# Kernel tuning notes

Hardware: AMD Instinct MI355X
Metric: run time of the kernel (lower is better)

The kernel has to match this reference:

```python
import jax, jax.numpy as jnp
import numpy as np

B, N, C, H, NC, P = 16, 577, 768, 12, 8, 576  # batch, seq(=patches+cls), dim, heads, curves, patches
D = C // H


def setup_inputs() -> dict:
    key = jax.random.key(0)
    ks = jax.random.split(key, 8)
    x = jax.random.normal(ks[0], (B, N, C), jnp.float32)
    qkv_w = jax.random.normal(ks[1], (C, 3 * C), jnp.float32) * 0.02
    proj_w = jax.random.normal(ks[2], (C, C), jnp.float32) * 0.02
    proj_b = jnp.zeros((C,), jnp.float32)
    # learned per-head decay logits; +3 so sigmoid ~0.95 (slow decay, realistic)
    ai_list = jax.random.normal(ks[3], (NC, H), jnp.float32) + 3.0
    mask_weights = jax.random.normal(ks[4], (NC,), jnp.float32) * 0.1 + 1.0 / NC
    normalize = 1.0 + 0.1 * jax.random.normal(ks[5], (H,), jnp.float32)
    # space-filling-curve inverse index permutations (one per curve)
    curve_inds = jnp.stack([
        jax.random.permutation(jax.random.fold_in(ks[6], c), P) for c in range(NC)
    ]).astype(jnp.int32)
    return dict(x=x, qkv_w=qkv_w, proj_w=proj_w, proj_b=proj_b,
                ai_list=ai_list, mask_weights=mask_weights,
                normalize=normalize, curve_inds=curve_inds)


def _build_mask(ai_list, mask_weights, curve_inds):
    # sigmoid(a)^|i-j| gathered by the curve permutation == sigmoid(a)^|ind_i - ind_j|
    a = jax.nn.sigmoid(ai_list)                                  # [NC,H]
    ci = curve_inds.astype(jnp.float32)                          # [NC,P]
    diff = jnp.abs(ci[:, :, None] - ci[:, None, :])              # [NC,P,P]
    Mc = a[:, :, None, None] ** diff[:, None, :, :]              # [NC,H,P,P]
    Mp = jnp.einsum('c,chpq->hpq', mask_weights, Mc)             # weighted sum over curves
    # cls-token row/col: each curve contributes ones -> sum of weights
    sw = jnp.sum(mask_weights)
    M = jnp.pad(Mp, ((0, 0), (1, 0), (1, 0)))                    # [H,N,N]
    M = M.at[:, 0, :].set(sw)
    M = M.at[:, :, 0].set(sw)
    return M


def reference(x, qkv_w, proj_w, proj_b, ai_list, mask_weights, normalize, curve_inds):
    qkv = (x @ qkv_w).reshape(B, N, 3, H, D)
    q = jnp.transpose(qkv[:, :, 0], (0, 2, 1, 3))                # [B,H,N,D]
    k = jnp.transpose(qkv[:, :, 1], (0, 2, 1, 3))
    v = jnp.transpose(qkv[:, :, 2], (0, 2, 1, 3))
    # NOTE: original overwrites self.scale with the bool `scale`=True -> multiply by 1
    attn = jnp.einsum('bhnd,bhmd->bhnm', q, k)                   # [B,H,N,N]
    M = _build_mask(ai_list, mask_weights, curve_inds)           # [H,N,N]
    attn = attn * M[None] * normalize[None, :, None, None]       # method='mul_v1'
    attn = jax.nn.softmax(attn, axis=-1)
    out = jnp.einsum('bhnm,bhmd->bhnd', attn, v)
    out = jnp.transpose(out, (0, 2, 1, 3)).reshape(B, N, C)
    return out @ proj_w + proj_b
```

## Files before the change

### kernel.cpp

```cpp
#include <hip/hip_runtime.h>


typedef _Float16 f16;
typedef _Float16 half8 __attribute__((ext_vector_type(8)));
typedef _Float16 half4 __attribute__((ext_vector_type(4)));
typedef float floatx4 __attribute__((ext_vector_type(4)));

#define DEVINL __device__ __forceinline__

#define Bb 16
#define NN 577
#define CC 768
#define HH 12
#define DD 64
#define MM (Bb * NN)
#define VTLD 584
#define MLD 580
#define CLD 136
#define TLD 264

DEVINL void async_copy16(void* lds, const void* g) {
  __builtin_amdgcn_global_load_lds(
      (const __attribute__((address_space(1))) void*)g,
      (__attribute__((address_space(3))) void*)lds, 16, 0, 0);
}

DEVINL half8 ld_swz(const f16* lds, int row, int chunk) {
  return *(const half8*)(lds + row * 64 + ((chunk ^ (row & 7)) << 3));
}

DEVINL int xcd_swizzle(int orig, int nwg) {
  int q = nwg >> 3, r = nwg & 7;
  int xcd = orig & 7, loc = orig >> 3;
  return (xcd < r ? xcd * (q + 1) : r * (q + 1) + (xcd - r) * q) + loc;
}

__global__ __launch_bounds__(256)
void prep_kernel(const float* __restrict__ x, const float* __restrict__ qkvw,
                 const float* __restrict__ pw, const float* __restrict__ ai,
                 const float* __restrict__ mw, const float* __restrict__ nrm,
                 const int* __restrict__ ci, f16* __restrict__ x_h,
                 f16* __restrict__ w_t, f16* __restrict__ pw_t,
                 float* __restrict__ Mb) {
  __shared__ float shm[32 * 33];
  const int bid = blockIdx.x;
  const int tid = threadIdx.x;
  if (bid < 6924) {
    int i = (bid * 256 + tid) * 4;
    float4 v = *(const float4*)(x + i);
    half4 o = {(f16)v.x, (f16)v.y, (f16)v.z, (f16)v.w};
    *(half4*)(x_h + i) = o;
  } else if (bid < 9228) {
    bool isq = bid < 8652;
    int b2 = bid - (isq ? 6924 : 8652);
    int N3 = isq ? 3 * CC : CC;
    const float* in = isq ? qkvw : pw;
    f16* out = isq ? w_t : pw_t;
    const int k0 = (b2 % 24) * 32, n0 = (b2 / 24) * 32;
    const int tx = tid & 31, ty = tid >> 5;
#pragma unroll
    for (int p = 0; p < 4; ++p)
      shm[(ty + p * 8) * 33 + tx] = in[(size_t)(k0 + ty + p * 8) * N3 + n0 + tx];
    __syncthreads();
#pragma unroll
    for (int p = 0; p < 4; ++p)
      out[(size_t)(n0 + ty + p * 8) * CC + k0 + tx] = (f16)shm[tx * 33 + ty + p * 8];
  } else {
    int b4 = bid - 9228;
    int i = b4 % NN, h = b4 / NN;
    float* la_s = shm; float* wv_s = shm + 8; float* cif = shm + 16;
    float* swn_s = shm + 24;
    if (tid < 8) {
      float av = ai[tid * 12 + h];
      float a = 1.f / (1.f + __expf(-av));
      la_s[tid] = __logf(a);
      wv_s[tid] = mw[tid];
      cif[tid] = (i > 0) ? (float)ci[tid * 576 + (i - 1)] : 0.f;
    }
    if (tid == 0) {
      float s = 0.f;
      for (int c = 0; c < 8; ++c) s += mw[c];
      swn_s[0] = s * nrm[h] * 1.44269504088896f;
    }
    __syncthreads();
    const float nr = nrm[h] * 1.44269504088896f;
    float* row = Mb + ((size_t)h * NN + i) * MLD;
    for (int j = tid; j < NN; j += 256) {
      float val;
      if (i == 0 || j == 0) {
        val = swn_s[0];
      } else {
        float acc = 0.f;
#pragma unroll
        for (int c = 0; c < 8; ++c) {
          float d = fabsf(cif[c] - (float)ci[c * 576 + (j - 1)]);
          acc += wv_s[c] * __expf(la_s[c] * d);
        }
        val = acc * nr;
      }
      row[j] = val;
    }
  }
}

DEVINL void gemm_mainloop(const f16* __restrict__ A, const f16* __restrict__ Bt,
                          int arow0, int brow0, int maxar,
                          f16* SMEM, floatx4 acc[4][4], int tid) {
  const int lane = tid & 63;
  const int wid = tid >> 6;
  const int wr = wid >> 1, wc = wid & 1;
  const int l15 = lane & 15, g = lane >> 4;
  const int r_ = tid >> 3, cp_ = tid & 7;
  const int lc_ = (cp_ ^ (r_ & 7)) << 3;

  auto stage = [&](f16* As, f16* Bs, int k0) {
#pragma unroll
    for (int q = 0; q < 4; ++q) {
      int r = q * 64 + r_;
      int ar = arow0 + r; if (ar > maxar) ar = maxar;
      async_copy16(As + (q * 512 + tid) * 8, A + (size_t)ar * CC + k0 + lc_);
    }
#pragma unroll
    for (int q = 0; q < 2; ++q) {
      int r = q * 64 + r_;
      async_copy16(Bs + (q * 512 + tid) * 8, Bt + (size_t)(brow0 + r) * CC + k0 + lc_);
    }
  };
  auto compute = [&](const f16* As, const f16* Bs) {
#pragma unroll
    for (int kk = 0; kk < 2; ++kk) {
      half8 af[4], bf[4];
#pragma unroll
      for (int mi = 0; mi < 4; ++mi) af[mi] = ld_swz(As, wr * 64 + mi * 16 + l15, kk * 4 + g);
#pragma unroll
      for (int ni = 0; ni < 4; ++ni) bf[ni] = ld_swz(Bs, wc * 64 + ni * 16 + l15, kk * 4 + g);
#pragma unroll
      for (int mi = 0; mi < 4; ++mi)
#pragma unroll
        for (int ni = 0; ni < 4; ++ni)
          acc[mi][ni] = __builtin_amdgcn_mfma_f32_16x16x32_f16(af[mi], bf[ni], acc[mi][ni], 0, 0, 0);
    }
  };

  const int nt = CC / 64;
  stage(SMEM, SMEM + 16384, 0);
#pragma unroll 1
  for (int t = 0; t < nt; ++t) {
    f16* cAs = (t & 1) ? SMEM + 24576 : SMEM;
    f16* cBs = (t & 1) ? SMEM + 40960 : SMEM + 16384;
    f16* nAs = (t & 1) ? SMEM : SMEM + 24576;
    f16* nBs = (t & 1) ? SMEM + 16384 : SMEM + 40960;
    if (t + 1 < nt) {
      stage(nAs, nBs, (t + 1) * 64);
      asm volatile("s_waitcnt vmcnt(6)" ::: "memory");
    } else {
      asm volatile("s_waitcnt vmcnt(0)" ::: "memory");
    }
    __builtin_amdgcn_s_barrier();
    __builtin_amdgcn_sched_barrier(0);
    compute(cAs, cBs);
    __builtin_amdgcn_s_barrier();
  }
}

__global__ __launch_bounds__(512, 2)
void gemm_qkv(const f16* __restrict__ A, const f16* __restrict__ Bt,
              f16* __restrict__ qb, f16* __restrict__ kb, f16* __restrict__ vt) {
  __shared__ __align__(16) f16 SMEM[49152];
  floatx4 acc[4][4] = {};
  const int nwg = 18 * 37;
  const int wgid = xcd_swizzle(blockIdx.y * gridDim.x + blockIdx.x, nwg);
  const int m0 = (wgid / 18) * 256, n0 = (wgid % 18) * 128;
  gemm_mainloop(A, Bt, m0, n0, MM - 1, SMEM, acc, threadIdx.x);
  const int tid = threadIdx.x, lane = tid & 63, wid = tid >> 6;
  const int wr = wid >> 1, wc = wid & 1, l15 = lane & 15, g = lane >> 4;
  const int t = n0 / CC;
  const int h0 = (n0 - t * CC) >> 6;
  if (t < 2) {
#pragma unroll
    for (int mi = 0; mi < 4; ++mi)
#pragma unroll
      for (int ni = 0; ni < 4; ++ni)
#pragma unroll
        for (int r = 0; r < 4; ++r)
          SMEM[(wr * 64 + mi * 16 + 4 * g + r) * CLD + wc * 64 + ni * 16 + l15] =
              (f16)acc[mi][ni][r];
    __syncthreads();
    f16* dst = (t == 0) ? qb : kb;
#pragma unroll
    for (int p = 0; p < 8; ++p) {
      int c = p * 512 + tid;
      int ml = c >> 4, n3c = (c & 15) << 3;
      int mg = m0 + ml;
      if (mg < MM) {
        int b = mg / NN, n = mg - b * NN;
        int h = h0 + (n3c >> 6), d0 = n3c & 63;
        half8 v = *(const half8*)(SMEM + ml * CLD + n3c);
        *(half8*)(dst + ((size_t)(b * HH + h) * NN + n) * DD + d0) = v;
      }
    }
  } else {
#pragma unroll
    for (int mi = 0; mi < 4; ++mi)
#pragma unroll
      for (int ni = 0; ni < 4; ++ni)
#pragma unroll
        for (int r = 0; r < 4; ++r)
          SMEM[(wc * 64 + ni * 16 + l15) * TLD + wr * 64 + mi * 16 + 4 * g + r] =
              (f16)acc[mi][ni][r];
    __syncthreads();
#pragma unroll
    for (int p = 0; p < 8; ++p) {
      int c = p * 512 + tid;
      int n3 = c >> 5, mc = (c & 31) << 3;
      int mg = m0 + mc;
      int h = h0 + (n3 >> 6), d = n3 & 63;
      half8 v = *(const half8*)(SMEM + n3 * TLD + mc);
      int b0 = mg / NN;
      if (mg + 7 < MM && (mg + 7) / NN == b0) {
        *(half8*)(vt + ((size_t)(b0 * HH + h) * DD + d) * VTLD + (mg - b0 * NN)) = v;
      } else {
#pragma unroll
        for (int e = 0; e < 8; ++e) {
          int m2 = mg + e;
          if (m2 < MM) {
            int b = m2 / NN;
            vt[((size_t)(b * HH + h) * DD + d) * VTLD + (m2 - b * NN)] = v[e];
          }
        }
      }
    }
  }
}

__global__ __launch_bounds__(512, 2)
void gemm_proj(const f16* __restrict__ A, const f16* __restrict__ Bt,
               const float* __restrict__ bias, float* __restrict__ out) {
  __shared__ __align__(16) f16 SMEM[49152];
  floatx4 acc[4][4] = {};
  const int nwg = 6 * 37;
  const int wgid = xcd_swizzle(blockIdx.y * gridDim.x + blockIdx.x, nwg);
  const int m0 = (wgid / 6) * 256, n0 = (wgid % 6) * 128;
  gemm_mainloop(A, Bt, m0, n0, MM - 1, SMEM, acc, threadIdx.x);
  const int lane = threadIdx.x & 63, wid = threadIdx.x >> 6;
  const int wr = wid >> 1, wc = wid & 1, l15 = lane & 15, g = lane >> 4;
#pragma unroll
  for (int mi = 0; mi < 4; ++mi)
#pragma unroll
    for (int ni = 0; ni < 4; ++ni)
#pragma unroll
      for (int r = 0; r < 4; ++r) {
        int m = m0 + wr * 64 + mi * 16 + 4 * g + r;
        if (m >= MM) continue;
        int n = n0 + wc * 64 + ni * 16 + l15;
        out[(size_t)m * CC + n] = acc[mi][ni][r] + bias[n];
      }
}

__global__ __launch_bounds__(512, 4)
void attn_kernel(const f16* __restrict__ qb, const f16* __restrict__ kb,
                 const f16* __restrict__ vt, const float* __restrict__ Mb,
                 f16* __restrict__ aout) {
  __shared__ f16 Ks[2][64 * 64];
  __shared__ f16 Vs[2][64 * 64];
  const int D0 = (blockIdx.z * gridDim.y + blockIdx.y) * gridDim.x + blockIdx.x;
  const int wgid = xcd_swizzle(D0, 5 * HH * Bb);
  const int it = wgid % 5;
  const int rem = wgid / 5;
  const int b = rem % Bb, h = rem / Bb;
  const int tid = threadIdx.x, lane = tid & 63, wid = tid >> 6;
  const int l15 = lane & 15, g = lane >> 4;
  const size_t bh = (size_t)b * HH + h;
  const f16* qbh = qb + bh * NN * DD;
  const f16* kbh = kb + bh * NN * DD;
  const f16* vbh = vt + bh * DD * VTLD;
  const float* Mh = Mb + (size_t)h * NN * MLD;
  const int row0w = it * 128 + wid * 16;

  half8 qB0, qB1;
  {
    int qr = row0w + l15; if (qr > NN - 1) qr = NN - 1;
    const f16* qp = qbh + (size_t)qr * DD + g * 8;
    qB0 = *(const half8*)qp;
    qB1 = *(const half8*)(qp + 32);
  }
  const float* Mrow;
  {
    int r0 = row0w + l15; if (r0 > NN - 1) r0 = NN - 1;
    Mrow = Mh + (size_t)r0 * MLD + 4 * g;
  }

  floatx4 acc[4] = {};
  float lsum = 0.f;
  float mrun = -3e38f;

  const int sr_ = tid >> 3, scp_ = tid & 7;
  const int slc_ = (scp_ ^ (sr_ & 7)) << 3;
  auto stage = [&](f16* Kd, f16* Vd, int j0) {
    int j = j0 + sr_; if (j > NN - 1) j = NN - 1;
    async_copy16(Kd + tid * 8, kbh + (size_t)j * DD + slc_);
    async_copy16(Vd + tid * 8, vbh + (size_t)sr_ * VTLD + j0 + slc_);
  };
  auto ldmask = [&](floatx4 m4[4], int j0) {
#pragma unroll
    for (int jt = 0; jt < 4; ++jt)
      m4[jt] = *(const floatx4*)(Mrow + j0 + jt * 16);
  };
  auto compute = [&](const f16* Kc, const f16* Vc, floatx4 m4[4], int j0) {
    floatx4 sf[4];
#pragma unroll
    for (int jt = 0; jt < 4; ++jt) {
      half8 ka0 = ld_swz(Kc, jt * 16 + l15, g);
      half8 ka1 = ld_swz(Kc, jt * 16 + l15, 4 + g);
      floatx4 z = {0.f, 0.f, 0.f, 0.f};
      z = __builtin_amdgcn_mfma_f32_16x16x32_f16(ka0, qB0, z, 0, 0, 0);
      z = __builtin_amdgcn_mfma_f32_16x16x32_f16(ka1, qB1, z, 0, 0, 0);
      sf[jt] = z;
    }
#pragma unroll
    for (int jt = 0; jt < 4; ++jt)
#pragma unroll
      for (int r = 0; r < 4; ++r) sf[jt][r] *= m4[jt][r];
    if (j0 + 64 > NN) {
#pragma unroll
      for (int jt = 0; jt < 4; ++jt)
#pragma unroll
        for (int r = 0; r < 4; ++r)
          if (j0 + jt * 16 + 4 * g + r >= NN) sf[jt][r] = -3e38f;
    }
    float pj[4];
#pragma unroll
    for (int jt = 0; jt < 4; ++jt)
      pj[jt] = fmaxf(fmaxf(sf[jt][0], sf[jt][1]), fmaxf(sf[jt][2], sf[jt][3]));
    float pmax_loc = fmaxf(fmaxf(pj[0], pj[1]), fmaxf(pj[2], pj[3]));
    if (__any(pmax_loc - mrun > 8.f)) {
      float pmax = fmaxf(pmax_loc, __shfl_xor(pmax_loc, 16));
      pmax = fmaxf(pmax, __shfl_xor(pmax, 32));
      float mnew = fmaxf(mrun, pmax);
      float fac = __builtin_amdgcn_exp2f(mrun - mnew);
      mrun = mnew;
      lsum *= fac;
#pragma unroll
      for (int dt = 0; dt < 4; ++dt)
#pragma unroll
        for (int r = 0; r < 4; ++r) acc[dt][r] *= fac;
    }
    half4 pB[4];
    float lsj[4];
#pragma unroll
    for (int jt = 0; jt < 4; ++jt) {
      half4 pb;
      float p0 = __builtin_amdgcn_exp2f(sf[jt][0] - mrun);
      float p1 = __builtin_amdgcn_exp2f(sf[jt][1] - mrun);
      float p2 = __builtin_amdgcn_exp2f(sf[jt][2] - mrun);
      float p3 = __builtin_amdgcn_exp2f(sf[jt][3] - mrun);
      pb[0] = (f16)p0; pb[1] = (f16)p1; pb[2] = (f16)p2; pb[3] = (f16)p3;
      lsj[jt] = (p0 + p1) + (p2 + p3);
      pB[jt] = pb;
    }
    lsum += (lsj[0] + lsj[1]) + (lsj[2] + lsj[3]);
#pragma unroll
    for (int dt = 0; dt < 4; ++dt)
#pragma unroll
      for (int jt = 0; jt < 4; ++jt) {
        int c16 = (jt * 2 + (g >> 1)) ^ (l15 & 7);
        half4 va = *(const half4*)(Vc + (dt * 16 + l15) * 64 + (c16 << 3) + (g & 1) * 4);
        acc[dt] = __builtin_amdgcn_mfma_f32_16x16x16f16(va, pB[jt], acc[dt], 0, 0, 0);
      }
  };

  floatx4 m4A[4], m4B[4];
  stage(Ks[0], Vs[0], 0);
  ldmask(m4A, 0);

#pragma unroll 1
  for (int t = 0; t < 10; t += 2) {
    ldmask(m4B, (t + 1) * 64);
    asm volatile("s_waitcnt vmcnt(4)" ::: "memory");
    __builtin_amdgcn_s_barrier();
    __builtin_amdgcn_sched_barrier(0);
    stage(Ks[1], Vs[1], (t + 1) * 64);
    compute(Ks[0], Vs[0], m4A, t * 64);
    const int j2 = (t + 2 < 10) ? (t + 2) * 64 : 0;
    ldmask(m4A, j2);
    asm volatile("s_waitcnt vmcnt(4)" ::: "memory");
    __builtin_amdgcn_s_barrier();
    __builtin_amdgcn_sched_barrier(0);
    stage(Ks[0], Vs[0], j2);
    compute(Ks[1], Vs[1], m4B, (t + 1) * 64);
  }

  {
    float v = lsum;
    v += __shfl_xor(v, 16);
    v += __shfl_xor(v, 32);
    float linv = 1.f / v;
    int n = row0w + l15;
    if (n < NN) {
#pragma unroll
      for (int dt = 0; dt < 4; ++dt) {
        half4 o;
#pragma unroll
        for (int r = 0; r < 4; ++r) o[r] = (f16)(acc[dt][r] * linv);
        *(half4*)(aout + ((size_t)(b * NN + n)) * CC + h * DD + dt * 16 + 4 * g) = o;
      }
    }
  }
}

extern "C" void kernel_launch(void* const* d_in, const int* in_sizes, int n_in,
                              void* d_out, int out_size, void* d_ws, size_t ws_size,
                              hipStream_t stream) {
  const float* x    = (const float*)d_in[0];
  const float* qkvw = (const float*)d_in[1];
  const float* pw   = (const float*)d_in[2];
  const float* pb   = (const float*)d_in[3];
  const float* ai   = (const float*)d_in[4];
  const float* mw   = (const float*)d_in[5];
  const float* nrm  = (const float*)d_in[6];
  const int*   ci   = (const int*)d_in[7];
  float* out = (float*)d_out;

  char* wsb = (char*)d_ws;
  size_t off = 0;
  auto alloc = [&](size_t bytes) {
    char* p = wsb + off;
    off += (bytes + 255) & ~(size_t)255;
    return p;
  };
  f16*   x_h  = (f16*)alloc((size_t)MM * CC * 2);
  f16*   w_t  = (f16*)alloc((size_t)3 * CC * CC * 2);
  f16*   pw_t = (f16*)alloc((size_t)CC * CC * 2);
  float* Mb   = (float*)alloc((size_t)HH * NN * MLD * 4 + 1024);
  f16*   qb   = (f16*)alloc((size_t)Bb * HH * NN * DD * 2);
  f16*   kb   = (f16*)alloc((size_t)Bb * HH * NN * DD * 2);
  f16*   vt   = (f16*)alloc((size_t)Bb * HH * DD * VTLD * 2);
  (void)alloc(4096);
  f16* aout = x_h;

  prep_kernel<<<16152, 256, 0, stream>>>(x, qkvw, pw, ai, mw, nrm, ci,
                                         x_h, w_t, pw_t, Mb);
  gemm_qkv<<<dim3(18, 37), 512, 0, stream>>>(x_h, w_t, qb, kb, vt);
  attn_kernel<<<dim3(5, HH, Bb), 512, 0, stream>>>(qb, kb, vt, Mb, aout);
  gemm_proj<<<dim3(6, 37), 512, 0, stream>>>(aout, pw_t, pb, out);
}
```

Before: 148.4 us.

## Triple-buffer GEMM mainloop and interleave split tile loads with MFMA halves

The shared GEMM mainloop for the QKV and projection kernels moves from a double buffer to a three-stage LDS ring, prefetching two K-tiles ahead. Each tile's global-to-LDS copy is split into two parts, each issued between the two MFMA half-steps, and MFMA sections run at raised wave priority via s_setprio. The aim is to hide global load latency and overlap LDS fragment reads with matrix math. In exchange, LDS use per block rises to about 147KB, which may limit occupancy, and each iteration adds barriers.

```diff
diff --git a/kernel.cpp b/kernel.cpp
--- a/kernel.cpp
+++ b/kernel.cpp
@@ -18,6 +18,7 @@
 #define MLD 580
 #define CLD 136
 #define TLD 264
+#define BUFS 24576
 
 DEVINL void async_copy16(void* lds, const void* g) {
   __builtin_amdgcn_global_load_lds(
@@ -113,52 +114,79 @@
   const int r_ = tid >> 3, cp_ = tid & 7;
   const int lc_ = (cp_ ^ (r_ & 7)) << 3;
 
-  auto stage = [&](f16* As, f16* Bs, int k0) {
-#pragma unroll
-    for (int q = 0; q < 4; ++q) {
+  auto stageA3 = [&](f16* As, int k0) {
+#pragma unroll
+    for (int q = 0; q < 3; ++q) {
       int r = q * 64 + r_;
       int ar = arow0 + r; if (ar > maxar) ar = maxar;
       async_copy16(As + (q * 512 + tid) * 8, A + (size_t)ar * CC + k0 + lc_);
     }
+  };
+  auto stageRest = [&](f16* As, f16* Bs, int k0) {
+    {
+      int r = 192 + r_;
+      int ar = arow0 + r; if (ar > maxar) ar = maxar;
+      async_copy16(As + (3 * 512 + tid) * 8, A + (size_t)ar * CC + k0 + lc_);
+    }
 #pragma unroll
     for (int q = 0; q < 2; ++q) {
       int r = q * 64 + r_;
       async_copy16(Bs + (q * 512 + tid) * 8, Bt + (size_t)(brow0 + r) * CC + k0 + lc_);
     }
   };
-  auto compute = [&](const f16* As, const f16* Bs) {
-#pragma unroll
-    for (int kk = 0; kk < 2; ++kk) {
-      half8 af[4], bf[4];
-#pragma unroll
-      for (int mi = 0; mi < 4; ++mi) af[mi] = ld_swz(As, wr * 64 + mi * 16 + l15, kk * 4 + g);
-#pragma unroll
-      for (int ni = 0; ni < 4; ++ni) bf[ni] = ld_swz(Bs, wc * 64 + ni * 16 + l15, kk * 4 + g);
-#pragma unroll
-      for (int mi = 0; mi < 4; ++mi)
-#pragma unroll
-        for (int ni = 0; ni < 4; ++ni)
-          acc[mi][ni] = __builtin_amdgcn_mfma_f32_16x16x32_f16(af[mi], bf[ni], acc[mi][ni], 0, 0, 0);
-    }
-  };
 
   const int nt = CC / 64;
-  stage(SMEM, SMEM + 16384, 0);
+  stageA3(SMEM, 0);
+  stageRest(SMEM, SMEM + 16384, 0);
+  stageA3(SMEM + BUFS, 64);
+  stageRest(SMEM + BUFS, SMEM + BUFS + 16384, 64);
+  asm volatile("s_waitcnt vmcnt(6)" ::: "memory");
+  __builtin_amdgcn_s_barrier();
+
 #pragma unroll 1
   for (int t = 0; t < nt; ++t) {
-    f16* cAs = (t & 1) ? SMEM + 24576 : SMEM;
-    f16* cBs = (t & 1) ? SMEM + 40960 : SMEM + 16384;
-    f16* nAs = (t & 1) ? SMEM : SMEM + 24576;
-    f16* nBs = (t & 1) ? SMEM + 16384 : SMEM + 40960;
-    if (t + 1 < nt) {
-      stage(nAs, nBs, (t + 1) * 64);
+    f16* cAs = SMEM + (t % 3) * BUFS;
+    f16* cBs = cAs + 16384;
+    f16* nAs = SMEM + ((t + 2) % 3) * BUFS;
+    f16* nBs = nAs + 16384;
+    const bool more = (t + 2 < nt);
+    half8 af[4], bf[4];
+#pragma unroll
+    for (int mi = 0; mi < 4; ++mi) af[mi] = ld_swz(cAs, wr * 64 + mi * 16 + l15, g);
+#pragma unroll
+    for (int ni = 0; ni < 4; ++ni) bf[ni] = ld_swz(cBs, wc * 64 + ni * 16 + l15, g);
+    if (more) stageA3(nAs, (t + 2) * 64);
+    __builtin_amdgcn_s_barrier();
+    asm volatile("s_waitcnt lgkmcnt(0)" ::: "memory");
+    __builtin_amdgcn_sched_barrier(0);
+    __builtin_amdgcn_s_setprio(1);
+#pragma unroll
+    for (int mi = 0; mi < 4; ++mi)
+#pragma unroll
+      for (int ni = 0; ni < 4; ++ni)
+        acc[mi][ni] = __builtin_amdgcn_mfma_f32_16x16x32_f16(af[mi], bf[ni], acc[mi][ni], 0, 0, 0);
+    __builtin_amdgcn_s_setprio(0);
+    __builtin_amdgcn_s_barrier();
+#pragma unroll
+    for (int mi = 0; mi < 4; ++mi) af[mi] = ld_swz(cAs, wr * 64 + mi * 16 + l15, 4 + g);
+#pragma unroll
+    for (int ni = 0; ni < 4; ++ni) bf[ni] = ld_swz(cBs, wc * 64 + ni * 16 + l15, 4 + g);
+    if (more) {
+      stageRest(nAs, nBs, (t + 2) * 64);
       asm volatile("s_waitcnt vmcnt(6)" ::: "memory");
-    } else {
+    } else if (t + 1 < nt) {
       asm volatile("s_waitcnt vmcnt(0)" ::: "memory");
     }
     __builtin_amdgcn_s_barrier();
+    asm volatile("s_waitcnt lgkmcnt(0)" ::: "memory");
     __builtin_amdgcn_sched_barrier(0);
-    compute(cAs, cBs);
+    __builtin_amdgcn_s_setprio(1);
+#pragma unroll
+    for (int mi = 0; mi < 4; ++mi)
+#pragma unroll
+      for (int ni = 0; ni < 4; ++ni)
+        acc[mi][ni] = __builtin_amdgcn_mfma_f32_16x16x32_f16(af[mi], bf[ni], acc[mi][ni], 0, 0, 0);
+    __builtin_amdgcn_s_setprio(0);
     __builtin_amdgcn_s_barrier();
   }
 }
@@ -166,7 +194,7 @@
 __global__ __launch_bounds__(512, 2)
 void gemm_qkv(const f16* __restrict__ A, const f16* __restrict__ Bt,
               f16* __restrict__ qb, f16* __restrict__ kb, f16* __restrict__ vt) {
-  __shared__ __align__(16) f16 SMEM[49152];
+  __shared__ __align__(16) f16 SMEM[3 * BUFS];
   floatx4 acc[4][4] = {};
   const int nwg = 18 * 37;
   const int wgid = xcd_swizzle(blockIdx.y * gridDim.x + blockIdx.x, nwg);
@@ -236,7 +264,7 @@
 __global__ __launch_bounds__(512, 2)
 void gemm_proj(const f16* __restrict__ A, const f16* __restrict__ Bt,
                const float* __restrict__ bias, float* __restrict__ out) {
-  __shared__ __align__(16) f16 SMEM[49152];
+  __shared__ __align__(16) f16 SMEM[3 * BUFS];
   floatx4 acc[4][4] = {};
   const int nwg = 6 * 37;
   const int wgid = xcd_swizzle(blockIdx.y * gridDim.x + blockIdx.x, nwg);
```

Result: slower. 152.8 us (+3.0%).
